# Performance work log

Hardware: AMD Instinct MI355X
Metric: run time of the kernel (lower is better)

Reference implementation:

```python
import jax, jax.numpy as jnp
import numpy as np

B, C1, C2, H, W = 3, 256, 256, 48, 48
CC = 128      # c = int(c2*e)
NB = 2        # n blocks
HEADS = 4     # max(1, 128//32)
HD = CC // HEADS
SCALE = HD ** -0.5
EPS = 1e-5


def setup_inputs():
    key = jax.random.key(0)
    ks = iter(jax.random.split(key, 64))
    def rn(shape, scale=1.0):
        return jax.random.normal(next(ks), shape, jnp.float32) * scale
    s1 = 1.0 / np.sqrt(C1)
    sc = 1.0 / np.sqrt(CC)
    s2c = 1.0 / np.sqrt(2 * CC)
    s4c = 1.0 / np.sqrt(4 * CC)
    inp = {
        'x': rn((B, C1, H, W)),
        'cv1_w': rn((2 * CC, C1), s1),
        'cv1_g': 1.0 + rn((2 * CC,), 0.1), 'cv1_b': rn((2 * CC,), 0.1),
        'cv1_m': rn((2 * CC,), 0.1), 'cv1_v': 1.0 + 0.5 * jax.random.uniform(next(ks), (2 * CC,)),
        'n1_g': 1.0 + rn((NB, CC), 0.1), 'n1_b': rn((NB, CC), 0.1),
        'qkv_w': rn((NB, 3 * CC, CC), sc), 'qkv_b': rn((NB, 3 * CC), 0.02),
        'proj_w': rn((NB, CC, CC), sc), 'proj_b': rn((NB, CC), 0.02),
        'n2_g': 1.0 + rn((NB, CC), 0.1), 'n2_b': rn((NB, CC), 0.1),
        'f1_w': rn((NB, 2 * CC, CC), sc), 'f1_b': rn((NB, 2 * CC), 0.02),
        'f2_w': rn((NB, CC, 2 * CC), s2c), 'f2_b': rn((NB, CC), 0.02),
        'cv2_w': rn((C2, 4 * CC), s4c),
        'cv2_g': 1.0 + rn((C2,), 0.1), 'cv2_b': rn((C2,), 0.1),
        'cv2_m': rn((C2,), 0.1), 'cv2_v': 1.0 + 0.5 * jax.random.uniform(next(ks), (C2,)),
    }
    return inp


def conv1x1(x, w, b=None):
    y = jnp.einsum('bchw,oc->bohw', x, w)
    if b is not None:
        y = y + b[:, None, None]
    return y


def conv_bn_silu(x, w, g, b, m, v):
    y = conv1x1(x, w)
    y = (y - m[:, None, None]) / jnp.sqrt(v + EPS)[:, None, None] * g[:, None, None] + b[:, None, None]
    return jax.nn.silu(y)


def groupnorm1(x, g, b):
    mu = x.mean(axis=(1, 2, 3), keepdims=True)
    var = x.var(axis=(1, 2, 3), keepdims=True)
    return (x - mu) / jnp.sqrt(var + EPS) * g[:, None, None] + b[:, None, None]


def attention(x, qw, qb, pw, pb):
    # Faithful to torch code incl. the unbind(0)-over-batch quirk (requires B==3).
    b, c, h, w = x.shape
    qkv = conv1x1(x, qw, qb)                                   # (3, 3C, H, W)
    qkv = qkv.reshape(b, 3, HEADS, HD, h * w)                  # (B=3, 3, heads, hd, HW)
    q, k, v = qkv[0], qkv[1], qkv[2]                           # each (3, heads, hd, HW)
    attn = jnp.einsum('ghdn,ghdm->ghnm', q, k) * SCALE         # q.T @ k -> (3, heads, HW, HW)
    attn = jax.nn.softmax(attn, axis=-1)
    out = jnp.einsum('ghdm,ghnm->ghdn', v, attn)               # v @ attn.T -> (3, heads, hd, HW)
    out = out.transpose(0, 2, 1, 3).reshape(b, c, h, w)        # transpose(1,2).reshape
    return conv1x1(out, pw, pb)


def forward(x, cv1_w, cv1_g, cv1_b, cv1_m, cv1_v, n1_g, n1_b, qkv_w, qkv_b,
            proj_w, proj_b, n2_g, n2_b, f1_w, f1_b, f2_w, f2_b,
            cv2_w, cv2_g, cv2_b, cv2_m, cv2_v):
    y = conv_bn_silu(x, cv1_w, cv1_g, cv1_b, cv1_m, cv1_v)     # (B, 2c, H, W)
    y1, y2 = y[:, :CC], y[:, CC:]
    outs = [y1, y2]
    cur = y2
    for i in range(NB):
        a = attention(groupnorm1(cur, n1_g[i], n1_b[i]), qkv_w[i], qkv_b[i], proj_w[i], proj_b[i])
        cur = cur + a
        h2 = groupnorm1(cur, n2_g[i], n2_b[i])
        f = jax.nn.gelu(conv1x1(h2, f1_w[i], f1_b[i]), approximate=False)
        cur = cur + conv1x1(f, f2_w[i], f2_b[i])
        outs.append(cur)
    cat = jnp.concatenate(outs, axis=1)                        # (B, 4c, H, W)
    return conv_bn_silu(cat, cv2_w, cv2_g, cv2_b, cv2_m, cv2_v)


def reference(x, cv1_w, cv1_g, cv1_b, cv1_m, cv1_v, n1_g, n1_b, qkv_w, qkv_b,
              proj_w, proj_b, n2_g, n2_b, f1_w, f1_b, f2_w, f2_b,
              cv2_w, cv2_g, cv2_b, cv2_m, cv2_v):
    return forward(x, cv1_w, cv1_g, cv1_b, cv1_m, cv1_v, n1_g, n1_b, qkv_w, qkv_b,
                   proj_w, proj_b, n2_g, n2_b, f1_w, f1_b, f2_w, f2_b,
                   cv2_w, cv2_g, cv2_b, cv2_m, cv2_v)
```

## Files before the change

### kernel.cpp

```cpp
#include <hip/hip_runtime.h>
#include <hip/hip_bf16.h>
#include <math.h>

#define HW 2304
#define EPSV 1e-5f
#define INV_N (1.f / 294912.f)
#define QS_LOG2E (0.17677669529663687f * 1.44269504088896340f)

enum { E_CV1 = 0, E_QKV = 1, E_RES = 2, E_F1 = 3, E_CV2 = 4 };

typedef __attribute__((ext_vector_type(8))) short bf16x8;
typedef __attribute__((ext_vector_type(4))) float f32x4;

static __device__ __forceinline__ ushort b16(float f) {
    union { __hip_bfloat16 h; ushort u; } cv;
    cv.h = __float2bfloat16(f);
    return cv.u;
}
static __device__ __forceinline__ float bf(ushort u) {
    union { unsigned u; float f; } c; c.u = (unsigned)u << 16; return c.f;
}
static __device__ __forceinline__ void stat_acc(float* STAT, int slot, int b,
                                                float s, float sq) {
    #pragma unroll
    for (int off = 32; off; off >>= 1) { s += __shfl_xor(s, off); sq += __shfl_xor(sq, off); }
    if ((threadIdx.x & 63) == 0) {
        atomicAdd(&STAT[(slot * 3 + b) * 2], s);
        atomicAdd(&STAT[(slot * 3 + b) * 2 + 1], sq);
    }
}

__global__ __launch_bounds__(256) void prep(
    const float* __restrict__ cv1w, const float* __restrict__ projw,
    const float* __restrict__ f2w, const float* __restrict__ cv2w,
    const float* __restrict__ qw, const float* __restrict__ g1, const float* __restrict__ b1,
    const float* __restrict__ fw1, const float* __restrict__ g2, const float* __restrict__ b2,
    const float* __restrict__ X,
    ushort* __restrict__ WB, ushort* __restrict__ FW, float* __restrict__ CV,
    ushort* __restrict__ XT, float* __restrict__ STAT)
{
    __shared__ ushort tb[64][68];
    const int bid = blockIdx.x, t = threadIdx.x;
    if (bid < 288) {
        if (bid == 0 && t < 32) STAT[t] = 0.f;
        const int idx = (bid * 256 + t) * 4;
        const float* src;
        int off;
        if      (idx < 65536)  { src = cv1w; off = 0; }
        else if (idx < 98304)  { src = projw; off = 65536; }
        else if (idx < 163840) { src = f2w;  off = 98304; }
        else                   { src = cv2w; off = 163840; }
        float4 v = *(const float4*)&src[idx - off];
        ushort4 u;
        u.x = b16(v.x); u.y = b16(v.y); u.z = b16(v.z); u.w = b16(v.w);
        *(ushort4*)&WB[idx] = u;
    } else if (bid < 293) {
        const int idx = (bid - 288) * 256 + t;
        if (idx >= 1280) return;
        const int i = idx / 640, r = idx % 640;
        float sw = 0.f, wb = 0.f;
        if (r < 384) {
            const float* wrow = qw + ((size_t)i * 384 + r) * 128;
            const float* gg = g1 + i * 128;
            const float* bb = b1 + i * 128;
            ushort* dst = FW + (size_t)i * 49152 + r * 128;
            for (int c = 0; c < 128; c++) {
                const float w = wrow[c], wp = w * gg[c];
                dst[c] = b16(wp); sw += wp; wb += w * bb[c];
            }
            CV[i * 1280 + r] = sw;
            CV[i * 1280 + 384 + r] = wb;
        } else {
            const int o = r - 384;
            const float* wrow = fw1 + ((size_t)i * 256 + o) * 128;
            const float* gg = g2 + i * 128;
            const float* bb = b2 + i * 128;
            ushort* dst = FW + 98304 + (size_t)i * 32768 + o * 128;
            for (int c = 0; c < 128; c++) {
                const float w = wrow[c], wp = w * gg[c];
                dst[c] = b16(wp); sw += wp; wb += w * bb[c];
            }
            CV[i * 1280 + 768 + o] = sw;
            CV[i * 1280 + 1024 + o] = wb;
        }
    } else {
        const int flat = bid - 293;
        const int bx = flat % 36, by = (flat / 36) % 4, bz = flat / 144;
        const int cb = by * 64, nb = bx * 64;
        #pragma unroll
        for (int k = 0; k < 4; k++) {
            const int row = k * 16 + (t >> 4), cq = t & 15;
            float4 v = *(const float4*)&X[(size_t)(bz * 256 + cb + row) * HW + nb + cq * 4];
            ushort4 u; u.x = b16(v.x); u.y = b16(v.y); u.z = b16(v.z); u.w = b16(v.w);
            *(ushort4*)&tb[row][cq * 4] = u;
        }
        __syncthreads();
        #pragma unroll
        for (int k = 0; k < 4; k++) {
            const int n = k * 16 + (t >> 4), cq = t & 15;
            ushort4 u;
            u.x = tb[cq * 4 + 0][n]; u.y = tb[cq * 4 + 1][n];
            u.z = tb[cq * 4 + 2][n]; u.w = tb[cq * 4 + 3][n];
            *(ushort4*)&XT[((size_t)bz * HW + nb + n) * 256 + cb + cq * 4] = u;
        }
    }
}

template <int EPI>
__global__ __launch_bounds__(256) void gemm_mfma(
    const ushort* __restrict__ W, const ushort* __restrict__ X,
    int K, int xld, int xoff,
    const float* __restrict__ q0, const float* __restrict__ q1,
    const float* __restrict__ q2, const float* __restrict__ q3,
    float* __restrict__ STAT, int slotUse, int slotAcc,
    const float* __restrict__ cvec,
    ushort* __restrict__ CT, int rcol, int ycol,
    float* __restrict__ Yf,
    ushort* __restrict__ U0, ushort* __restrict__ U1, ushort* __restrict__ U2)
{
    const int b = blockIdx.z;
    const int t = threadIdx.x;
    const int w = t >> 6, l = t & 63;
    const int ln = l & 15, lg = l >> 4;
    const int wo = (w & 1) * 64, wn = (w >> 1) * 64;
    const int ob = blockIdx.y * 128 + wo;
    const int nb = blockIdx.x * 128 + wn;

    const ushort* ap = W + (size_t)(ob + ln) * K + lg * 8;
    const ushort* bp = X + ((size_t)b * HW + nb + ln) * xld + xoff + lg * 8;

    bf16x8 a0[4], bb0[4], a1[4], bb1[4];
    #pragma unroll
    for (int i = 0; i < 4; i++) {
        a0[i]  = *(const bf16x8*)(ap + (size_t)i * 16 * K);
        bb0[i] = *(const bf16x8*)(bp + (size_t)i * 16 * xld);
    }
    f32x4 acc[4][4];
    #pragma unroll
    for (int i = 0; i < 4; i++)
        #pragma unroll
        for (int j = 0; j < 4; j++) acc[i][j] = (f32x4){0.f, 0.f, 0.f, 0.f};

    for (int c0 = 32; c0 <= K; c0 += 32) {
        if (c0 < K) {
            #pragma unroll
            for (int i = 0; i < 4; i++) {
                a1[i]  = *(const bf16x8*)(ap + (size_t)i * 16 * K + c0);
                bb1[i] = *(const bf16x8*)(bp + (size_t)i * 16 * xld + c0);
            }
        }
        #pragma unroll
        for (int i = 0; i < 4; i++)
            #pragma unroll
            for (int j = 0; j < 4; j++)
                acc[i][j] = __builtin_amdgcn_mfma_f32_16x16x32_bf16(a0[i], bb0[j], acc[i][j], 0, 0, 0);
        #pragma unroll
        for (int i = 0; i < 4; i++) { a0[i] = a1[i]; bb0[i] = bb1[i]; }
    }

    float mu = 0.f, rs = 0.f;
    if (EPI == E_QKV || EPI == E_F1) {
        const float s  = STAT[(slotUse * 3 + b) * 2];
        const float sq = STAT[(slotUse * 3 + b) * 2 + 1];
        mu = s * INV_N;
        rs = rsqrtf(sq * INV_N - mu * mu + EPSV);
    }
    float ls = 0.f, lsq = 0.f;

    #pragma unroll
    for (int i = 0; i < 4; i++) {
        const int obase = ob + i * 16 + lg * 4;
        if (EPI == E_CV1 || EPI == E_CV2) {
            float sc[4], sh[4];
            #pragma unroll
            for (int r = 0; r < 4; r++) {
                const int o = obase + r;
                const float irs = rsqrtf(q3[o] + EPSV);
                sc[r] = q0[o] * irs;
                sh[r] = q1[o] - q2[o] * sc[r];
            }
            #pragma unroll
            for (int j = 0; j < 4; j++) {
                const int n = nb + j * 16 + ln;
                ushort4 u;
                #pragma unroll
                for (int r = 0; r < 4; r++) {
                    float y = fmaf(acc[i][j][r], sc[r], sh[r]);
                    y = y / (1.f + __expf(-y));
                    if (EPI == E_CV2) {
                        Yf[(size_t)(b * 256 + obase + r) * HW + n] = y;
                    } else {
                        ls += y; lsq += y * y;
                        if (r == 0) u.x = b16(y); else if (r == 1) u.y = b16(y);
                        else if (r == 2) u.z = b16(y); else u.w = b16(y);
                    }
                }
                if (EPI == E_CV1)
                    *(ushort4*)&CT[((size_t)b * HW + n) * 512 + ycol + obase] = u;
            }
        } else if (EPI == E_QKV) {
            const int gh = obase >> 5;
            const int d0 = obase & 31;
            float C[4];
            #pragma unroll
            for (int r = 0; r < 4; r++) {
                const int o = obase + r;
                C[r] = q0[o] + cvec[384 + o] - rs * mu * cvec[o];
            }
            #pragma unroll
            for (int j = 0; j < 4; j++) {
                const int n = nb + j * 16 + ln;
                float y0 = fmaf(rs, acc[i][j][0], C[0]);
                float y1 = fmaf(rs, acc[i][j][1], C[1]);
                float y2 = fmaf(rs, acc[i][j][2], C[2]);
                float y3 = fmaf(rs, acc[i][j][3], C[3]);
                if (b == 0) {
                    ushort4 u;
                    u.x = b16(y0 * QS_LOG2E); u.y = b16(y1 * QS_LOG2E);
                    u.z = b16(y2 * QS_LOG2E); u.w = b16(y3 * QS_LOG2E);
                    *(ushort4*)&U0[((size_t)gh * HW + n) * 32 + d0] = u;
                } else if (b == 1) {
                    ushort4 u;
                    u.x = b16(y0); u.y = b16(y1); u.z = b16(y2); u.w = b16(y3);
                    *(ushort4*)&U1[((size_t)gh * HW + n) * 32 + d0] = u;
                } else {
                    U2[(size_t)(obase + 0) * HW + n] = b16(y0);
                    U2[(size_t)(obase + 1) * HW + n] = b16(y1);
                    U2[(size_t)(obase + 2) * HW + n] = b16(y2);
                    U2[(size_t)(obase + 3) * HW + n] = b16(y3);
                }
            }
        } else if (EPI == E_RES) {
            #pragma unroll
            for (int j = 0; j < 4; j++) {
                const int n = nb + j * 16 + ln;
                const size_t base = ((size_t)b * HW + n) * 512;
                ushort4 rv = *(const ushort4*)&CT[base + rcol + obase];
                float y0 = acc[i][j][0] + q0[obase + 0] + bf(rv.x);
                float y1 = acc[i][j][1] + q0[obase + 1] + bf(rv.y);
                float y2 = acc[i][j][2] + q0[obase + 2] + bf(rv.z);
                float y3 = acc[i][j][3] + q0[obase + 3] + bf(rv.w);
                ls += (y0 + y1) + (y2 + y3);
                lsq += y0 * y0 + y1 * y1 + y2 * y2 + y3 * y3;
                ushort4 u;
                u.x = b16(y0); u.y = b16(y1); u.z = b16(y2); u.w = b16(y3);
                *(ushort4*)&CT[base + ycol + obase] = u;
            }
        } else {
            float C[4];
            #pragma unroll
            for (int r = 0; r < 4; r++) {
                const int o = obase + r;
                C[r] = q0[o] + cvec[256 + o] - rs * mu * cvec[o];
            }
            #pragma unroll
            for (int j = 0; j < 4; j++) {
                const int n = nb + j * 16 + ln;
                ushort4 u;
                #pragma unroll
                for (int r = 0; r < 4; r++) {
                    float y = fmaf(rs, acc[i][j][r], C[r]);
                    y = 0.5f * y * (1.f + erff(y * 0.70710678f));
                    if (r == 0) u.x = b16(y); else if (r == 1) u.y = b16(y);
                    else if (r == 2) u.z = b16(y); else u.w = b16(y);
                }
                *(ushort4*)&U0[((size_t)b * HW + n) * 256 + obase] = u;
            }
        }
    }
    if (EPI == E_CV1 && slotAcc >= 0 && blockIdx.y == 1) stat_acc(STAT, slotAcc, b, ls, lsq);
    if (EPI == E_RES && slotAcc >= 0) stat_acc(STAT, slotAcc, b, ls, lsq);
}

__global__ __launch_bounds__(256) void attn_mfma(
    const ushort* __restrict__ QT,
    const ushort* __restrict__ KT,
    const ushort* __restrict__ VB,
    float* __restrict__ PO0, float* __restrict__ PO1,
    float* __restrict__ PO2, float* __restrict__ PO3,
    float* __restrict__ MS)
{
    __shared__ __align__(16) ushort Kl[2][2048];
    __shared__ __align__(16) ushort Vl[2][2048];
    __shared__ __align__(16) ushort plds[4][16][72];
    const int gh = blockIdx.y, g = gh >> 2, h = gh & 3;
    const int half = blockIdx.z;
    const int t = threadIdx.x, w = t >> 6, l = t & 63;
    const int ln = l & 15, lg = l >> 4;
    const int n0 = (blockIdx.x * 4 + w) * 16;
    const int ms0 = half * 576, mend = ms0 + 576;

    const ushort* ktg = KT + (size_t)gh * HW * 32;
    const ushort* vg  = VB + ((size_t)g * 128 + h * 32) * HW;

    const int krow = t >> 2, kcq = t & 3;
    const int vrow = t >> 3, vcq = t & 7;
    const int kw = krow * 32 + ((kcq ^ (krow & 3)) << 3);
    const int vw = vrow * 64 + ((vcq ^ (vrow & 7)) << 3);
    const int krd = ln * 32 + ((lg ^ (ln & 3)) << 3);
    const int vs  = ln & 7;
    const int vrd0 = ln * 64 + ((lg ^ vs) << 3);
    const int vrd1 = ln * 64 + (((lg + 4) ^ vs) << 3);
    const int vrd2 = (16 + ln) * 64 + ((lg ^ vs) << 3);
    const int vrd3 = (16 + ln) * 64 + (((lg + 4) ^ vs) << 3);

    const bf16x8 qf = *(const bf16x8*)(QT + ((size_t)gh * HW + n0 + ln) * 32 + lg * 8);

    f32x4 o0 = {0.f, 0.f, 0.f, 0.f}, o1 = {0.f, 0.f, 0.f, 0.f};
    float M = -3.0e38f, S = 0.f;

    {
        bf16x8 kr = *(const bf16x8*)(ktg + (size_t)(ms0 + krow) * 32 + kcq * 8);
        bf16x8 vr = *(const bf16x8*)(vg + (size_t)vrow * HW + ms0 + vcq * 8);
        *(bf16x8*)&Kl[0][kw] = kr;
        *(bf16x8*)&Vl[0][vw] = vr;
    }
    int cur = 0;

    for (int m0 = ms0; m0 < mend; m0 += 64) {
        __syncthreads();
        const bool more = (m0 + 64 < mend);
        bf16x8 kr, vr;
        if (more) {
            kr = *(const bf16x8*)(ktg + (size_t)(m0 + 64 + krow) * 32 + kcq * 8);
            vr = *(const bf16x8*)(vg + (size_t)vrow * HW + m0 + 64 + vcq * 8);
        }

        f32x4 st[4];
        const f32x4 zero = {0.f, 0.f, 0.f, 0.f};
        #pragma unroll
        for (int mc = 0; mc < 4; mc++) {
            const bf16x8 kf = *(const bf16x8*)&Kl[cur][mc * 512 + krd];
            st[mc] = __builtin_amdgcn_mfma_f32_16x16x32_bf16(kf, qf, zero, 0, 0, 0);
        }

        float mx = st[0][0];
        #pragma unroll
        for (int mc = 0; mc < 4; mc++)
            #pragma unroll
            for (int r = 0; r < 4; r++) mx = fmaxf(mx, st[mc][r]);
        mx = fmaxf(mx, __shfl_xor(mx, 16));
        mx = fmaxf(mx, __shfl_xor(mx, 32));
        if (!__all(mx <= M + 8.f)) {
            const float Mn = fmaxf(M, mx);
            const float corr = exp2f(M - Mn);
            S *= corr;
            #pragma unroll
            for (int r = 0; r < 4; r++) { o0[r] *= corr; o1[r] *= corr; }
            M = Mn;
        }
        float ps = 0.f;
        ushort4 pw[4];
        #pragma unroll
        for (int mc = 0; mc < 4; mc++) {
            float p0v = exp2f(st[mc][0] - M), p1v = exp2f(st[mc][1] - M);
            float p2v = exp2f(st[mc][2] - M), p3v = exp2f(st[mc][3] - M);
            ps += (p0v + p1v) + (p2v + p3v);
            pw[mc].x = b16(p0v); pw[mc].y = b16(p1v);
            pw[mc].z = b16(p2v); pw[mc].w = b16(p3v);
        }
        ps += __shfl_xor(ps, 16);
        ps += __shfl_xor(ps, 32);
        S += ps;

        #pragma unroll
        for (int mc = 0; mc < 4; mc++)
            *(ushort4*)&plds[w][ln][mc * 16 + lg * 4] = pw[mc];
        bf16x8 pf0 = *(const bf16x8*)&plds[w][ln][lg * 8];
        bf16x8 pf1 = *(const bf16x8*)&plds[w][ln][32 + lg * 8];

        const bf16x8 vf0 = *(const bf16x8*)&Vl[cur][vrd0];
        const bf16x8 vf1 = *(const bf16x8*)&Vl[cur][vrd1];
        const bf16x8 vf2 = *(const bf16x8*)&Vl[cur][vrd2];
        const bf16x8 vf3 = *(const bf16x8*)&Vl[cur][vrd3];
        o0 = __builtin_amdgcn_mfma_f32_16x16x32_bf16(vf0, pf0, o0, 0, 0, 0);
        o0 = __builtin_amdgcn_mfma_f32_16x16x32_bf16(vf1, pf1, o0, 0, 0, 0);
        o1 = __builtin_amdgcn_mfma_f32_16x16x32_bf16(vf2, pf0, o1, 0, 0, 0);
        o1 = __builtin_amdgcn_mfma_f32_16x16x32_bf16(vf3, pf1, o1, 0, 0, 0);

        if (more) {
            *(bf16x8*)&Kl[cur ^ 1][kw] = kr;
            *(bf16x8*)&Vl[cur ^ 1][vw] = vr;
        }
        cur ^= 1;
    }

    float* po = (half == 0) ? PO0 : (half == 1) ? PO1 : (half == 2) ? PO2 : PO3;
    #pragma unroll
    for (int r = 0; r < 4; r++) {
        const int d = lg * 4 + r;
        po[((size_t)gh * 32 + d) * HW + n0 + ln]      = o0[r];
        po[((size_t)gh * 32 + d + 16) * HW + n0 + ln] = o1[r];
    }
    if (lg == 0) {
        float* ms = MS + (((size_t)half * 12 + gh) * HW + n0 + ln) * 2;
        ms[0] = M; ms[1] = S;
    }
}

__global__ __launch_bounds__(256) void merge_proj(
    const float* __restrict__ PO0, const float* __restrict__ PO1,
    const float* __restrict__ PO2, const float* __restrict__ PO3,
    const float* __restrict__ MS,
    const ushort* __restrict__ PW, const float* __restrict__ pb,
    ushort* __restrict__ CT, int rcol, int ycol,
    float* __restrict__ STAT, int slotAcc)
{
    __shared__ float fw[4][4][64];
    __shared__ __align__(16) unsigned long long obuf[64][34];
    const int g = blockIdx.y, nb = blockIdx.x * 64;
    const int t = threadIdx.x;
    {
        const int h = t >> 6, nl = t & 63, gh = g * 4 + h, n = nb + nl;
        float Mk[4], Sk[4];
        #pragma unroll
        for (int k = 0; k < 4; k++) {
            Mk[k] = MS[(((size_t)k * 12 + gh) * HW + n) * 2 + 0];
            Sk[k] = MS[(((size_t)k * 12 + gh) * HW + n) * 2 + 1];
        }
        const float Mx = fmaxf(fmaxf(Mk[0], Mk[1]), fmaxf(Mk[2], Mk[3]));
        float wk[4], den = 0.f;
        #pragma unroll
        for (int k = 0; k < 4; k++) { wk[k] = exp2f(Mk[k] - Mx); den += Sk[k] * wk[k]; }
        const float inv = 1.f / den;
        #pragma unroll
        for (int k = 0; k < 4; k++) fw[h][k][nl] = wk[k] * inv;
    }
    __syncthreads();
    {
        const int nl = t & 63, dd = t >> 6;
        #pragma unroll
        for (int p = 0; p < 8; p++) {
            const int d = p * 4 + dd;
            ushort uu[4];
            #pragma unroll
            for (int h = 0; h < 4; h++) {
                const int gh = g * 4 + h;
                const size_t idx = ((size_t)gh * 32 + d) * HW + nb + nl;
                const float v = PO0[idx] * fw[h][0][nl] + PO1[idx] * fw[h][1][nl]
                              + PO2[idx] * fw[h][2][nl] + PO3[idx] * fw[h][3][nl];
                uu[h] = b16(v);
            }
            obuf[nl][d] = (unsigned long long)uu[0] | ((unsigned long long)uu[1] << 16)
                        | ((unsigned long long)uu[2] << 32) | ((unsigned long long)uu[3] << 48);
        }
    }
    __syncthreads();
    const int w = t >> 6, l = t & 63, ln = l & 15, lg = l >> 4;
    const int wo = (w & 1) * 64, wn = (w >> 1) * 32;
    const ushort* ob_base = (const ushort*)&obuf[0][0];
    const ushort* ap = PW + (size_t)(wo + ln) * 128 + lg * 8;
    f32x4 acc[4][2];
    #pragma unroll
    for (int i = 0; i < 4; i++)
        #pragma unroll
        for (int jf = 0; jf < 2; jf++) acc[i][jf] = (f32x4){0.f, 0.f, 0.f, 0.f};
    #pragma unroll
    for (int kk = 0; kk < 4; kk++) {
        bf16x8 bfr[2];
        #pragma unroll
        for (int jf = 0; jf < 2; jf++)
            bfr[jf] = *(const bf16x8*)(ob_base + (wn + jf * 16 + ln) * 136 + kk * 32 + lg * 8);
        #pragma unroll
        for (int i = 0; i < 4; i++) {
            const bf16x8 af = *(const bf16x8*)(ap + (size_t)i * 16 * 128 + kk * 32);
            acc[i][0] = __builtin_amdgcn_mfma_f32_16x16x32_bf16(af, bfr[0], acc[i][0], 0, 0, 0);
            acc[i][1] = __builtin_amdgcn_mfma_f32_16x16x32_bf16(af, bfr[1], acc[i][1], 0, 0, 0);
        }
    }
    float ls = 0.f, lsq = 0.f;
    #pragma unroll
    for (int i = 0; i < 4; i++) {
        const int o4 = wo + i * 16 + lg * 4;
        #pragma unroll
        for (int jf = 0; jf < 2; jf++) {
            const int n = nb + wn + jf * 16 + ln;
            const size_t base = ((size_t)g * HW + n) * 512;
            ushort4 rv = *(const ushort4*)&CT[base + rcol + o4];
            float y0 = acc[i][jf][0] + pb[o4 + 0] + bf(rv.x);
            float y1 = acc[i][jf][1] + pb[o4 + 1] + bf(rv.y);
            float y2 = acc[i][jf][2] + pb[o4 + 2] + bf(rv.z);
            float y3 = acc[i][jf][3] + pb[o4 + 3] + bf(rv.w);
            ls += (y0 + y1) + (y2 + y3);
            lsq += y0 * y0 + y1 * y1 + y2 * y2 + y3 * y3;
            ushort4 u;
            u.x = b16(y0); u.y = b16(y1); u.z = b16(y2); u.w = b16(y3);
            *(ushort4*)&CT[base + ycol + o4] = u;
        }
    }
    stat_acc(STAT, slotAcc, g, ls, lsq);
}

extern "C" void kernel_launch(void* const* d_in, const int* in_sizes, int n_in,
                              void* d_out, int out_size, void* d_ws, size_t ws_size,
                              hipStream_t stream)
{
    (void)in_sizes; (void)n_in; (void)out_size; (void)ws_size;
    const float* x      = (const float*)d_in[0];
    const float* cv1_w  = (const float*)d_in[1];
    const float* cv1_g  = (const float*)d_in[2];
    const float* cv1_b  = (const float*)d_in[3];
    const float* cv1_m  = (const float*)d_in[4];
    const float* cv1_v  = (const float*)d_in[5];
    const float* n1_g   = (const float*)d_in[6];
    const float* n1_b   = (const float*)d_in[7];
    const float* qkv_w  = (const float*)d_in[8];
    const float* qkv_b  = (const float*)d_in[9];
    const float* proj_w = (const float*)d_in[10];
    const float* proj_b = (const float*)d_in[11];
    const float* n2_g   = (const float*)d_in[12];
    const float* n2_b   = (const float*)d_in[13];
    const float* f1_w   = (const float*)d_in[14];
    const float* f1_b   = (const float*)d_in[15];
    const float* f2_w   = (const float*)d_in[16];
    const float* f2_b   = (const float*)d_in[17];
    const float* cv2_w  = (const float*)d_in[18];
    const float* cv2_g  = (const float*)d_in[19];
    const float* cv2_b  = (const float*)d_in[20];
    const float* cv2_m  = (const float*)d_in[21];
    const float* cv2_v  = (const float*)d_in[22];
    float* out = (float*)d_out;

    float* ws = (float*)d_ws;
    ushort* CATT = (ushort*)ws;
    ushort* QT   = (ushort*)(ws + 1769472);
    ushort* KTb  = (ushort*)(ws + 2211840);
    ushort* VB   = (ushort*)(ws + 2654208);
    float*  MS   = ws + 3096576;
    ushort* WB   = (ushort*)(ws + 3317760);
    ushort* FW   = (ushort*)(ws + 3465216);
    float*  CV   = ws + 3547136;
    float*  STAT = ws + 3549696;
    float*  PO2  = ws + 3549760;
    float*  PO3  = PO2 + 884736;
    ushort* FT   = QT;
    ushort* XTX  = (ushort*)PO2;
    float*  PO0  = (float*)d_out;
    float*  PO1  = PO0 + 884736;

    dim3 blk(256);

    prep<<<dim3(725), blk, 0, stream>>>(
        cv1_w, proj_w, f2_w, cv2_w, qkv_w, n1_g, n1_b, f1_w, n2_g, n2_b,
        x, WB, FW, CV, XTX, STAT);

    gemm_mfma<E_CV1><<<dim3(18, 2, 3), blk, 0, stream>>>(
        WB + 0, XTX, 256, 256, 0, cv1_g, cv1_b, cv1_m, cv1_v,
        STAT, -1, 0, nullptr, CATT, 0, 0, nullptr, nullptr, nullptr, nullptr);

    for (int i = 0; i < 2; i++) {
        const int prev = (i == 0) ? 128 : 256;
        const int next = 256 + 128 * i;
        const int gn1 = (i == 0) ? 0 : 2;
        const int gn2 = (i == 0) ? 1 : 3;

        gemm_mfma<E_QKV><<<dim3(18, 3, 3), blk, 0, stream>>>(
            FW + (size_t)i * 49152, CATT, 128, 512, prev, qkv_b + i * 384,
            nullptr, nullptr, nullptr, STAT, gn1, -1, CV + i * 1280,
            nullptr, 0, 0, nullptr, QT, KTb, VB);
        attn_mfma<<<dim3(36, 12, 4), blk, 0, stream>>>(QT, KTb, VB, PO0, PO1, PO2, PO3, MS);
        merge_proj<<<dim3(36, 3), blk, 0, stream>>>(
            PO0, PO1, PO2, PO3, MS, WB + 65536 + (size_t)i * 16384, proj_b + i * 128,
            CATT, prev, next, STAT, gn2);

        gemm_mfma<E_F1><<<dim3(18, 2, 3), blk, 0, stream>>>(
            FW + 98304 + (size_t)i * 32768, CATT, 128, 512, next, f1_b + i * 256,
            nullptr, nullptr, nullptr, STAT, gn2, -1, CV + i * 1280 + 768,
            nullptr, 0, 0, nullptr, FT, nullptr, nullptr);
        gemm_mfma<E_RES><<<dim3(18, 1, 3), blk, 0, stream>>>(
            WB + 98304 + (size_t)i * 32768, FT, 256, 256, 0, f2_b + i * 128,
            nullptr, nullptr, nullptr, STAT, -1, (i == 0) ? 2 : -1, nullptr,
            CATT, next, next, nullptr, nullptr, nullptr, nullptr);
    }

    gemm_mfma<E_CV2><<<dim3(18, 2, 3), blk, 0, stream>>>(
        WB + 163840, CATT, 512, 512, 0, cv2_g, cv2_b, cv2_m, cv2_v,
        STAT, -1, -1, nullptr, nullptr, 0, 0, out, nullptr, nullptr, nullptr);
}
```

Measured before the change: 232.4 us.

## Split attention KV range six ways and load K/V directly into registers

Raises the attention split-K factor from 4 to 6 so more blocks run concurrently, and replaces the LDS double-buffered K/V staging and its block barrier with per-lane direct global loads into registers, prefetching the next K tile. The merge kernel now combines six partial outputs, and the workspace layout is reshuffled to hold the extra partial buffers. The cost is more partial-output traffic and merge work, plus uncoalesced and redundant global reads of K/V across waves that rely on cache.

```diff
diff --git a/kernel.cpp b/kernel.cpp
--- a/kernel.cpp
+++ b/kernel.cpp
@@ -6,6 +6,7 @@
 #define EPSV 1e-5f
 #define INV_N (1.f / 294912.f)
 #define QS_LOG2E (0.17677669529663687f * 1.44269504088896340f)
+#define NSPLIT 6
 
 enum { E_CV1 = 0, E_QKV = 1, E_RES = 2, E_F1 = 3, E_CV2 = 4 };
 
@@ -276,62 +277,46 @@
     const ushort* __restrict__ QT,
     const ushort* __restrict__ KT,
     const ushort* __restrict__ VB,
-    float* __restrict__ PO0, float* __restrict__ PO1,
-    float* __restrict__ PO2, float* __restrict__ PO3,
+    float* __restrict__ POa,
+    float* __restrict__ POb,
     float* __restrict__ MS)
 {
-    __shared__ __align__(16) ushort Kl[2][2048];
-    __shared__ __align__(16) ushort Vl[2][2048];
     __shared__ __align__(16) ushort plds[4][16][72];
     const int gh = blockIdx.y, g = gh >> 2, h = gh & 3;
-    const int half = blockIdx.z;
+    const int sp = blockIdx.z;
     const int t = threadIdx.x, w = t >> 6, l = t & 63;
     const int ln = l & 15, lg = l >> 4;
     const int n0 = (blockIdx.x * 4 + w) * 16;
-    const int ms0 = half * 576, mend = ms0 + 576;
-
-    const ushort* ktg = KT + (size_t)gh * HW * 32;
-    const ushort* vg  = VB + ((size_t)g * 128 + h * 32) * HW;
-
-    const int krow = t >> 2, kcq = t & 3;
-    const int vrow = t >> 3, vcq = t & 7;
-    const int kw = krow * 32 + ((kcq ^ (krow & 3)) << 3);
-    const int vw = vrow * 64 + ((vcq ^ (vrow & 7)) << 3);
-    const int krd = ln * 32 + ((lg ^ (ln & 3)) << 3);
-    const int vs  = ln & 7;
-    const int vrd0 = ln * 64 + ((lg ^ vs) << 3);
-    const int vrd1 = ln * 64 + (((lg + 4) ^ vs) << 3);
-    const int vrd2 = (16 + ln) * 64 + ((lg ^ vs) << 3);
-    const int vrd3 = (16 + ln) * 64 + (((lg + 4) ^ vs) << 3);
+    const int ms0 = sp * 384, mend = ms0 + 384;
 
     const bf16x8 qf = *(const bf16x8*)(QT + ((size_t)gh * HW + n0 + ln) * 32 + lg * 8);
+
+    const ushort* ktp = KT + (size_t)gh * HW * 32 + ln * 32 + lg * 8;
+    const ushort* vp0 = VB + ((size_t)g * 128 + h * 32 + ln) * HW + lg * 8;
+    const ushort* vp1 = vp0 + (size_t)16 * HW;
 
     f32x4 o0 = {0.f, 0.f, 0.f, 0.f}, o1 = {0.f, 0.f, 0.f, 0.f};
     float M = -3.0e38f, S = 0.f;
 
-    {
-        bf16x8 kr = *(const bf16x8*)(ktg + (size_t)(ms0 + krow) * 32 + kcq * 8);
-        bf16x8 vr = *(const bf16x8*)(vg + (size_t)vrow * HW + ms0 + vcq * 8);
-        *(bf16x8*)&Kl[0][kw] = kr;
-        *(bf16x8*)&Vl[0][vw] = vr;
-    }
-    int cur = 0;
+    bf16x8 kf[4], kfn[4], vf[4];
+    #pragma unroll
+    for (int mc = 0; mc < 4; mc++)
+        kf[mc] = *(const bf16x8*)(ktp + (size_t)(ms0 + mc * 16) * 32);
 
     for (int m0 = ms0; m0 < mend; m0 += 64) {
-        __syncthreads();
-        const bool more = (m0 + 64 < mend);
-        bf16x8 kr, vr;
-        if (more) {
-            kr = *(const bf16x8*)(ktg + (size_t)(m0 + 64 + krow) * 32 + kcq * 8);
-            vr = *(const bf16x8*)(vg + (size_t)vrow * HW + m0 + 64 + vcq * 8);
-        }
+        vf[0] = *(const bf16x8*)(vp0 + m0);  vf[1] = *(const bf16x8*)(vp0 + m0 + 32);
+        vf[2] = *(const bf16x8*)(vp1 + m0);  vf[3] = *(const bf16x8*)(vp1 + m0 + 32);
 
         f32x4 st[4];
         const f32x4 zero = {0.f, 0.f, 0.f, 0.f};
         #pragma unroll
-        for (int mc = 0; mc < 4; mc++) {
-            const bf16x8 kf = *(const bf16x8*)&Kl[cur][mc * 512 + krd];
-            st[mc] = __builtin_amdgcn_mfma_f32_16x16x32_bf16(kf, qf, zero, 0, 0, 0);
+        for (int mc = 0; mc < 4; mc++)
+            st[mc] = __builtin_amdgcn_mfma_f32_16x16x32_bf16(kf[mc], qf, zero, 0, 0, 0);
+
+        if (m0 + 64 < mend) {
+            #pragma unroll
+            for (int mc = 0; mc < 4; mc++)
+                kfn[mc] = *(const bf16x8*)(ktp + (size_t)(m0 + 64 + mc * 16) * 32);
         }
 
         float mx = st[0][0];
@@ -369,23 +354,17 @@
         bf16x8 pf0 = *(const bf16x8*)&plds[w][ln][lg * 8];
         bf16x8 pf1 = *(const bf16x8*)&plds[w][ln][32 + lg * 8];
 
-        const bf16x8 vf0 = *(const bf16x8*)&Vl[cur][vrd0];
-        const bf16x8 vf1 = *(const bf16x8*)&Vl[cur][vrd1];
-        const bf16x8 vf2 = *(const bf16x8*)&Vl[cur][vrd2];
-        const bf16x8 vf3 = *(const bf16x8*)&Vl[cur][vrd3];
-        o0 = __builtin_amdgcn_mfma_f32_16x16x32_bf16(vf0, pf0, o0, 0, 0, 0);
-        o0 = __builtin_amdgcn_mfma_f32_16x16x32_bf16(vf1, pf1, o0, 0, 0, 0);
-        o1 = __builtin_amdgcn_mfma_f32_16x16x32_bf16(vf2, pf0, o1, 0, 0, 0);
-        o1 = __builtin_amdgcn_mfma_f32_16x16x32_bf16(vf3, pf1, o1, 0, 0, 0);
-
-        if (more) {
-            *(bf16x8*)&Kl[cur ^ 1][kw] = kr;
-            *(bf16x8*)&Vl[cur ^ 1][vw] = vr;
-        }
-        cur ^= 1;
-    }
-
-    float* po = (half == 0) ? PO0 : (half == 1) ? PO1 : (half == 2) ? PO2 : PO3;
+        o0 = __builtin_amdgcn_mfma_f32_16x16x32_bf16(vf[0], pf0, o0, 0, 0, 0);
+        o0 = __builtin_amdgcn_mfma_f32_16x16x32_bf16(vf[1], pf1, o0, 0, 0, 0);
+        o1 = __builtin_amdgcn_mfma_f32_16x16x32_bf16(vf[2], pf0, o1, 0, 0, 0);
+        o1 = __builtin_amdgcn_mfma_f32_16x16x32_bf16(vf[3], pf1, o1, 0, 0, 0);
+
+        #pragma unroll
+        for (int mc = 0; mc < 4; mc++) kf[mc] = kfn[mc];
+    }
+
+    float* po = (sp < 2) ? (POa + (size_t)sp * 884736)
+                         : (POb + (size_t)(sp - 2) * 884736);
     #pragma unroll
     for (int r = 0; r < 4; r++) {
         const int d = lg * 4 + r;
@@ -393,38 +372,39 @@
         po[((size_t)gh * 32 + d + 16) * HW + n0 + ln] = o1[r];
     }
     if (lg == 0) {
-        float* ms = MS + (((size_t)half * 12 + gh) * HW + n0 + ln) * 2;
+        float* ms = MS + (((size_t)sp * 12 + gh) * HW + n0 + ln) * 2;
         ms[0] = M; ms[1] = S;
     }
 }
 
 __global__ __launch_bounds__(256) void merge_proj(
-    const float* __restrict__ PO0, const float* __restrict__ PO1,
-    const float* __restrict__ PO2, const float* __restrict__ PO3,
+    const float* __restrict__ POa, const float* __restrict__ POb,
     const float* __restrict__ MS,
     const ushort* __restrict__ PW, const float* __restrict__ pb,
     ushort* __restrict__ CT, int rcol, int ycol,
     float* __restrict__ STAT, int slotAcc)
 {
-    __shared__ float fw[4][4][64];
+    __shared__ float fw[4][NSPLIT][64];
     __shared__ __align__(16) unsigned long long obuf[64][34];
     const int g = blockIdx.y, nb = blockIdx.x * 64;
     const int t = threadIdx.x;
     {
         const int h = t >> 6, nl = t & 63, gh = g * 4 + h, n = nb + nl;
-        float Mk[4], Sk[4];
-        #pragma unroll
-        for (int k = 0; k < 4; k++) {
+        float Mk[NSPLIT], Sk[NSPLIT];
+        #pragma unroll
+        for (int k = 0; k < NSPLIT; k++) {
             Mk[k] = MS[(((size_t)k * 12 + gh) * HW + n) * 2 + 0];
             Sk[k] = MS[(((size_t)k * 12 + gh) * HW + n) * 2 + 1];
         }
-        const float Mx = fmaxf(fmaxf(Mk[0], Mk[1]), fmaxf(Mk[2], Mk[3]));
-        float wk[4], den = 0.f;
-        #pragma unroll
-        for (int k = 0; k < 4; k++) { wk[k] = exp2f(Mk[k] - Mx); den += Sk[k] * wk[k]; }
+        float Mx = Mk[0];
+        #pragma unroll
+        for (int k = 1; k < NSPLIT; k++) Mx = fmaxf(Mx, Mk[k]);
+        float wk[NSPLIT], den = 0.f;
+        #pragma unroll
+        for (int k = 0; k < NSPLIT; k++) { wk[k] = exp2f(Mk[k] - Mx); den += Sk[k] * wk[k]; }
         const float inv = 1.f / den;
         #pragma unroll
-        for (int k = 0; k < 4; k++) fw[h][k][nl] = wk[k] * inv;
+        for (int k = 0; k < NSPLIT; k++) fw[h][k][nl] = wk[k] * inv;
     }
     __syncthreads();
     {
@@ -437,8 +417,13 @@
             for (int h = 0; h < 4; h++) {
                 const int gh = g * 4 + h;
                 const size_t idx = ((size_t)gh * 32 + d) * HW + nb + nl;
-                const float v = PO0[idx] * fw[h][0][nl] + PO1[idx] * fw[h][1][nl]
-                              + PO2[idx] * fw[h][2][nl] + PO3[idx] * fw[h][3][nl];
+                float v = 0.f;
+                #pragma unroll
+                for (int k = 0; k < 2; k++)
+                    v += POa[(size_t)k * 884736 + idx] * fw[h][k][nl];
+                #pragma unroll
+                for (int k = 0; k < 4; k++)
+                    v += POb[(size_t)k * 884736 + idx] * fw[h][k + 2][nl];
                 uu[h] = b16(v);
             }
             obuf[nl][d] = (unsigned long long)uu[0] | ((unsigned long long)uu[1] << 16)
@@ -527,16 +512,14 @@
     ushort* KTb  = (ushort*)(ws + 2211840);
     ushort* VB   = (ushort*)(ws + 2654208);
     float*  MS   = ws + 3096576;
-    ushort* WB   = (ushort*)(ws + 3317760);
-    ushort* FW   = (ushort*)(ws + 3465216);
-    float*  CV   = ws + 3547136;
-    float*  STAT = ws + 3549696;
-    float*  PO2  = ws + 3549760;
-    float*  PO3  = PO2 + 884736;
+    ushort* WB   = (ushort*)(ws + 3428352);
+    ushort* FW   = (ushort*)(ws + 3575808);
+    float*  CV   = ws + 3657728;
+    float*  STAT = ws + 3660288;
+    float*  POb  = ws + 3660352;
     ushort* FT   = QT;
-    ushort* XTX  = (ushort*)PO2;
-    float*  PO0  = (float*)d_out;
-    float*  PO1  = PO0 + 884736;
+    ushort* XTX  = (ushort*)POb;
+    float*  POa  = (float*)d_out;
 
     dim3 blk(256);
 
@@ -558,9 +541,9 @@
             FW + (size_t)i * 49152, CATT, 128, 512, prev, qkv_b + i * 384,
             nullptr, nullptr, nullptr, STAT, gn1, -1, CV + i * 1280,
             nullptr, 0, 0, nullptr, QT, KTb, VB);
-        attn_mfma<<<dim3(36, 12, 4), blk, 0, stream>>>(QT, KTb, VB, PO0, PO1, PO2, PO3, MS);
+        attn_mfma<<<dim3(36, 12, NSPLIT), blk, 0, stream>>>(QT, KTb, VB, POa, POb, MS);
         merge_proj<<<dim3(36, 3), blk, 0, stream>>>(
-            PO0, PO1, PO2, PO3, MS, WB + 65536 + (size_t)i * 16384, proj_b + i * 128,
+            POa, POb, MS, WB + 65536 + (size_t)i * 16384, proj_b + i * 128,
             CATT, prev, next, STAT, gn2);
 
         gemm_mfma<E_F1><<<dim3(18, 2, 3), blk, 0, stream>>>(
```

After: 279.5 us. 1.2x slower.
